# Performance work log

Measured on AMD Instinct MI355X. Metric: run time of the kernel, lower is better.

Reference implementation:

```python
import jax, jax.numpy as jnp
import numpy as np

EMB = 192
HEADS = 6
WIN = (8, 8)
N = WIN[0] * WIN[1]  # 64
B_ = 2048
NW = 1024  # mask windows per image; B_ % NW == 0


def _relative_position_index():
    coords_h = np.arange(WIN[0])
    coords_w = np.arange(WIN[1])
    coords = np.stack(np.meshgrid(coords_h, coords_w, indexing='ij'))  # (2,Wh,Ww)
    cf = coords.reshape(2, -1)
    rel = cf[:, :, None] - cf[:, None, :]  # (2,N,N)
    rel = rel.transpose(1, 2, 0)
    rel[:, :, 0] += WIN[0] - 1
    rel[:, :, 1] += WIN[1] - 1
    rel[:, :, 0] *= 2 * WIN[1] - 1
    return rel.sum(-1).astype(np.int32)  # (N,N)


def setup_inputs() -> dict:
    key = jax.random.key(0)
    ks = jax.random.split(key, 12)
    num_bias = (2 * WIN[0] - 1) * (2 * WIN[1] - 1)  # 225
    s = 0.02
    return {
        'q': jax.random.normal(ks[0], (B_, N, EMB), jnp.float32),
        'k': jax.random.normal(ks[1], (B_, N, EMB), jnp.float32),
        'v': jax.random.normal(ks[2], (B_, N, EMB), jnp.float32),
        'mask': jax.random.normal(ks[3], (NW, N, N), jnp.float32),
        'Wq': jax.random.normal(ks[4], (EMB, EMB), jnp.float32) * s,
        'bq': jnp.zeros((EMB,), jnp.float32),
        'Wk': jax.random.normal(ks[5], (EMB, EMB), jnp.float32) * s,
        'bk': jnp.zeros((EMB,), jnp.float32),
        'Wv': jax.random.normal(ks[6], (EMB, EMB), jnp.float32) * s,
        'bv': jnp.zeros((EMB,), jnp.float32),
        'Wp': jax.random.normal(ks[7], (EMB, EMB), jnp.float32) * s,
        'bp': jnp.zeros((EMB,), jnp.float32),
        'bias_table': jax.random.normal(ks[8], (num_bias, HEADS), jnp.float32) * s,
        'rel_index': jnp.asarray(_relative_position_index()),
    }


def reference(q, k, v, mask, Wq, bq, Wk, bk, Wv, bv, Wp, bp, bias_table, rel_index):
    head_dim = EMB // HEADS
    scale = head_dim ** -0.5

    def split_heads(x):
        # (B_,N,C) -> (B_,H,N,D)
        return x.reshape(B_, N, HEADS, head_dim).transpose(0, 2, 1, 3)

    qh = split_heads(q @ Wq + bq) * scale
    kh = split_heads(k @ Wk + bk)
    vh = split_heads(v @ Wv + bv)

    attn = jnp.einsum('bhnd,bhmd->bhnm', qh, kh)  # (B_,H,N,N)

    # gathered relative position bias: (N,N,H) -> (H,N,N)
    rel_bias = bias_table[rel_index.reshape(-1)].reshape(N, N, HEADS).transpose(2, 0, 1)
    attn = attn + rel_bias[None]

    # mask add: reshape to (B, nW, H, N, N) and broadcast mask over batch/heads
    nW = mask.shape[0]
    attn = attn.reshape(-1, nW, HEADS, N, N) + mask[None, :, None]
    attn = attn.reshape(-1, HEADS, N, N)
    attn = jax.nn.softmax(attn, axis=-1)

    x = jnp.einsum('bhnm,bhmd->bhnd', attn, vh)  # (B_,H,N,D)
    x = x.transpose(0, 2, 1, 3).reshape(B_, N, EMB)
    x = x @ Wp + bp
    return (x, attn)
```

## Files before the change

kernel.cpp:

```cpp
#include <hip/hip_runtime.h>
#include <hip/hip_bf16.h>

typedef __attribute__((ext_vector_type(8))) short   bf16x8;
typedef __attribute__((ext_vector_type(4))) float   f32x4;
typedef unsigned short u16;

#define NTOK 64
#define CEMB 192
#define NH   6
#define ROWB 384
#define VROWB 128

__device__ __forceinline__ u16 f2b(float f) {
  unsigned u = __float_as_uint(f);
  unsigned r = (u + 0x7fffu + ((u >> 16) & 1u)) >> 16;
  return (u16)r;
}

__device__ __forceinline__ unsigned cvtpk(float lo, float hi) {
  unsigned r;
  asm("v_cvt_pk_bf16_f32 %0, %1, %2" : "=v"(r) : "v"(lo), "v"(hi));
  return r;
}

__device__ __forceinline__ int swz(int row, int colbyte) {
  return colbyte ^ ((((row >> 3) ^ row) & 7) << 4);
}

__global__ void prep_kernel(const float* __restrict__ Wq, const float* __restrict__ Wk,
                            const float* __restrict__ Wv, const float* __restrict__ Wp,
                            const float* __restrict__ btab, const int* __restrict__ ridx,
                            u16* __restrict__ WT, float* __restrict__ rb) {
  int idx = blockIdx.x * 256 + threadIdx.x;
  if (idx < 4 * 36864) {
    int m = idx / 36864;
    int e = idx - m * 36864;
    int n = e / CEMB;
    int k = e - n * CEMB;
    const float* W = (m == 0) ? Wq : (m == 1) ? Wk : (m == 2) ? Wv : Wp;
    WT[idx] = f2b(W[k * CEMB + n]);
  } else {
    int i2 = idx - 4 * 36864;
    if (i2 < NH * 4096) {
      int h = i2 >> 12;
      int ij = i2 & 4095;
      rb[i2] = btab[ridx[ij] * NH + h];
    }
  }
}

__global__ __launch_bounds__(512, 4)
void wattn_kernel(const float* __restrict__ qg, const float* __restrict__ kg,
                  const float* __restrict__ vg, const float* __restrict__ maskg,
                  const float* __restrict__ bq, const float* __restrict__ bk,
                  const float* __restrict__ bv, const float* __restrict__ bp,
                  const u16* __restrict__ WT, const float* __restrict__ rb,
                  float* __restrict__ xout, float* __restrict__ attn_out) {
  __shared__ __align__(16) char smem[81920];
  char* sQ = smem;
  char* sK = smem + 24576;
  char* sV = smem + 49152;
  const int tid  = threadIdx.x;
  const int wave = tid >> 6;
  const int lane = tid & 63;
  const int l15  = lane & 15;
  const int lhi  = lane >> 4;
  char* sP = smem + 73728 + wave * 1024;
  const int b = blockIdx.x;
  const float scale = 0.17677669529663687f;

  {
    const size_t base = (size_t)b * NTOK * CEMB;
    #pragma unroll
    for (int m = 0; m < 3; ++m) {
      const float* src = (m == 0 ? qg : m == 1 ? kg : vg) + base;
      char* dst = (m == 0 ? sQ : m == 1 ? sK : sV);
      #pragma unroll
      for (int it = 0; it < 6; ++it) {
        int fi  = it * 512 + tid;
        int row = fi / 48;
        int ce  = (fi - row * 48) * 4;
        const float4 v4 = reinterpret_cast<const float4*>(src)[fi];
        uint2 w;
        w.x = cvtpk(v4.x, v4.y);
        w.y = cvtpk(v4.z, v4.w);
        *reinterpret_cast<uint2*>(dst + row * ROWB + swz(row, ce * 2)) = w;
      }
    }
  }
  __syncthreads();

  #pragma unroll
  for (int m = 0; m < 3; ++m) {
    const char* Xs = (m == 0) ? sQ : (m == 1) ? sK : sV;
    const float* bias = (m == 0) ? bq : (m == 1) ? bk : bv;
    f32x4 acc[2][4];
    #pragma unroll
    for (int si = 0; si < 2; ++si) {
      int strip = wave + si * 8;
      if (strip < 12) {
        const u16* Wt = WT + m * 36864 + (strip * 16 + l15) * CEMB + lhi * 8;
        #pragma unroll
        for (int rt = 0; rt < 4; ++rt) { f32x4 z = {0.f,0.f,0.f,0.f}; acc[si][rt] = z; }
        #pragma unroll
        for (int ks = 0; ks < 6; ++ks) {
          bf16x8 bw = *reinterpret_cast<const bf16x8*>(Wt + ks * 32);
          #pragma unroll
          for (int rt = 0; rt < 4; ++rt) {
            int row = rt * 16 + l15;
            bf16x8 ax = *reinterpret_cast<const bf16x8*>(Xs + row * ROWB + swz(row, ks * 64 + lhi * 16));
            acc[si][rt] = __builtin_amdgcn_mfma_f32_16x16x32_bf16(ax, bw, acc[si][rt], 0, 0, 0);
          }
        }
      }
    }
    __syncthreads();
    #pragma unroll
    for (int si = 0; si < 2; ++si) {
      int strip = wave + si * 8;
      if (strip < 12) {
        int c = strip * 16 + l15;
        float bval = bias[c];
        if (m == 0) {
          #pragma unroll
          for (int rt = 0; rt < 4; ++rt)
            #pragma unroll
            for (int r = 0; r < 4; ++r) {
              int row = rt * 16 + lhi * 4 + r;
              *reinterpret_cast<u16*>(sQ + row * ROWB + swz(row, c * 2)) = f2b((acc[si][rt][r] + bval) * scale);
            }
        } else if (m == 1) {
          #pragma unroll
          for (int rt = 0; rt < 4; ++rt)
            #pragma unroll
            for (int r = 0; r < 4; ++r) {
              int row = rt * 16 + lhi * 4 + r;
              *reinterpret_cast<u16*>(sK + row * ROWB + swz(row, c * 2)) = f2b(acc[si][rt][r] + bval);
            }
        } else {
          #pragma unroll
          for (int rt = 0; rt < 4; ++rt) {
            int t0 = rt * 16 + lhi * 4;
            uint2 w;
            w.x = cvtpk(acc[si][rt][0] + bval, acc[si][rt][1] + bval);
            w.y = cvtpk(acc[si][rt][2] + bval, acc[si][rt][3] + bval);
            *reinterpret_cast<uint2*>(sV + c * VROWB + swz(c, t0 * 2)) = w;
          }
        }
      }
    }
  }
  __syncthreads();

  const float* maskw = maskg + (size_t)(b & 1023) * 4096;
  const int rt   = wave & 3;
  const int qrow = rt * 16 + l15;
  const int irow = rt * 16 + lhi * 4;

  f32x4 mk4[4];
  #pragma unroll
  for (int ct = 0; ct < 4; ++ct)
    mk4[ct] = *reinterpret_cast<const f32x4*>(maskw + qrow * 64 + ct * 16 + lhi * 4);

  #pragma unroll
  for (int ui = 0; ui < 3; ++ui) {
    int u = wave + ui * 8;
    int h = u >> 2;

    f32x4 rb4[4];
    #pragma unroll
    for (int ct = 0; ct < 4; ++ct)
      rb4[ct] = *reinterpret_cast<const f32x4*>(rb + h * 4096 + qrow * 64 + ct * 16 + lhi * 4);

    bf16x8 aq = *reinterpret_cast<const bf16x8*>(sQ + qrow * ROWB + swz(qrow, h * 64 + lhi * 16));
    f32x4 sv[4];
    #pragma unroll
    for (int ct = 0; ct < 4; ++ct) {
      int krow = ct * 16 + l15;
      bf16x8 bkf = *reinterpret_cast<const bf16x8*>(sK + krow * ROWB + swz(krow, h * 64 + lhi * 16));
      f32x4 z = {0.f, 0.f, 0.f, 0.f};
      sv[ct] = __builtin_amdgcn_mfma_f32_16x16x32_bf16(bkf, aq, z, 0, 0, 0);
    }

    float lg[4][4];
    #pragma unroll
    for (int ct = 0; ct < 4; ++ct)
      #pragma unroll
      for (int r = 0; r < 4; ++r)
        lg[ct][r] = sv[ct][r] + rb4[ct][r] + mk4[ct][r];

    float mx = fmaxf(fmaxf(fmaxf(lg[0][0], lg[0][1]), fmaxf(lg[0][2], lg[0][3])),
                     fmaxf(fmaxf(lg[1][0], lg[1][1]), fmaxf(lg[1][2], lg[1][3])));
    mx = fmaxf(mx, fmaxf(fmaxf(fmaxf(lg[2][0], lg[2][1]), fmaxf(lg[2][2], lg[2][3])),
                         fmaxf(fmaxf(lg[3][0], lg[3][1]), fmaxf(lg[3][2], lg[3][3]))));
    mx = fmaxf(mx, __shfl_xor(mx, 16));
    mx = fmaxf(mx, __shfl_xor(mx, 32));

    float e[4][4];
    float sum = 0.f;
    #pragma unroll
    for (int ct = 0; ct < 4; ++ct)
      #pragma unroll
      for (int r = 0; r < 4; ++r) {
        e[ct][r] = __expf(lg[ct][r] - mx);
        sum += e[ct][r];
      }
    sum += __shfl_xor(sum, 16);
    sum += __shfl_xor(sum, 32);
    float inv = 1.0f / sum;

    float pr[4][4];
    #pragma unroll
    for (int ct = 0; ct < 4; ++ct)
      #pragma unroll
      for (int r = 0; r < 4; ++r)
        pr[ct][r] = e[ct][r] * inv;

    float* ap = attn_out + ((size_t)b * NH + h) * 4096 + qrow * 64;
    #pragma unroll
    for (int ct = 0; ct < 4; ++ct) {
      f32x4 p4;
      p4[0] = pr[ct][0]; p4[1] = pr[ct][1]; p4[2] = pr[ct][2]; p4[3] = pr[ct][3];
      *reinterpret_cast<f32x4*>(ap + ct * 16 + lhi * 4) = p4;
    }

    f32x4 xa[2];
    { f32x4 z = {0.f, 0.f, 0.f, 0.f}; xa[0] = z; xa[1] = z; }
    #pragma unroll
    for (int ks = 0; ks < 2; ++ks) {
      #pragma unroll
      for (int c = 0; c < 2; ++c) {
        int ct = ks * 2 + c;
        int kg = c * 2 + (lhi >> 1);
        uint2 w;
        w.x = cvtpk(pr[ct][0], pr[ct][1]);
        w.y = cvtpk(pr[ct][2], pr[ct][3]);
        *reinterpret_cast<uint2*>(sP + (kg * 16 + l15) * 16 + (lhi & 1) * 8) = w;
      }
      bf16x8 apf = *reinterpret_cast<const bf16x8*>(sP + lane * 16);
      #pragma unroll
      for (int ctv = 0; ctv < 2; ++ctv) {
        int vrow = h * 32 + ctv * 16 + l15;
        bf16x8 bvf = *reinterpret_cast<const bf16x8*>(sV + vrow * VROWB + swz(vrow, ks * 64 + lhi * 16));
        xa[ctv] = __builtin_amdgcn_mfma_f32_16x16x32_bf16(apf, bvf, xa[ctv], 0, 0, 0);
      }
    }

    #pragma unroll
    for (int ctv = 0; ctv < 2; ++ctv)
      #pragma unroll
      for (int r = 0; r < 4; ++r) {
        int xrow = irow + r;
        int xcol = h * 32 + ctv * 16 + l15;
        *reinterpret_cast<u16*>(sQ + xrow * ROWB + swz(xrow, xcol * 2)) = f2b(xa[ctv][r]);
      }
  }
  __syncthreads();

  #pragma unroll
  for (int ui = 0; ui < 3; ++ui) {
    int u2 = wave + ui * 8;
    int ct = u2 % 12;
    int rh = u2 / 12;
    const u16* Wt = WT + 3 * 36864 + (ct * 16 + l15) * CEMB + lhi * 8;
    f32x4 oa[2];
    { f32x4 z = {0.f, 0.f, 0.f, 0.f}; oa[0] = z; oa[1] = z; }
    #pragma unroll
    for (int ks = 0; ks < 6; ++ks) {
      bf16x8 bw = *reinterpret_cast<const bf16x8*>(Wt + ks * 32);
      #pragma unroll
      for (int rr = 0; rr < 2; ++rr) {
        int xrow = rh * 32 + rr * 16 + l15;
        bf16x8 ax = *reinterpret_cast<const bf16x8*>(sQ + xrow * ROWB + swz(xrow, ks * 64 + lhi * 16));
        oa[rr] = __builtin_amdgcn_mfma_f32_16x16x32_bf16(ax, bw, oa[rr], 0, 0, 0);
      }
    }
    float bias = bp[ct * 16 + l15];
    #pragma unroll
    for (int rr = 0; rr < 2; ++rr)
      #pragma unroll
      for (int r = 0; r < 4; ++r)
        xout[((size_t)b * NTOK + rh * 32 + rr * 16 + lhi * 4 + r) * CEMB + ct * 16 + l15] = oa[rr][r] + bias;
  }
}

extern "C" void kernel_launch(void* const* d_in, const int* in_sizes, int n_in,
                              void* d_out, int out_size, void* d_ws, size_t ws_size,
                              hipStream_t stream) {
  const float* q    = (const float*)d_in[0];
  const float* k    = (const float*)d_in[1];
  const float* v    = (const float*)d_in[2];
  const float* mask = (const float*)d_in[3];
  const float* Wq   = (const float*)d_in[4];
  const float* bq   = (const float*)d_in[5];
  const float* Wk   = (const float*)d_in[6];
  const float* bk   = (const float*)d_in[7];
  const float* Wv   = (const float*)d_in[8];
  const float* bv   = (const float*)d_in[9];
  const float* Wp   = (const float*)d_in[10];
  const float* bp   = (const float*)d_in[11];
  const float* btab = (const float*)d_in[12];
  const int*   ridx = (const int*)d_in[13];

  u16*   WT = (u16*)d_ws;
  float* rb = (float*)((char*)d_ws + 4 * 36864 * 2);

  float* xout = (float*)d_out;
  float* attn = xout + (size_t)2048 * NTOK * CEMB;

  prep_kernel<<<672, 256, 0, stream>>>(Wq, Wk, Wv, Wp, btab, ridx, WT, rb);
  wattn_kernel<<<2048, 512, 0, stream>>>(q, k, v, mask, bq, bk, bv, bp, WT, rb, xout, attn);
}
```

Baseline: 214.0 us.

## Shrink LDS to two buffers, keep Q in registers, drop P scratch

Reorganizes the fused window-attention kernel so that LDS drops from three Q/K/V buffers plus per-wave P scratch to two 24KB buffers. Q is projected transposed straight into registers as bf16 fragments, and K is prefetched into registers and staged after Q. Scores and P·V now use 16x16x16 MFMAs, so the P fragments come straight from the accumulator layout without an LDS round trip. The aim is higher occupancy (launch bounds raised to 6) and fewer LDS writes, at the cost of extra barriers, including one inside the head loop, and more register pressure.

```diff
diff --git a/kernel.cpp b/kernel.cpp
--- a/kernel.cpp
+++ b/kernel.cpp
@@ -2,6 +2,7 @@
 #include <hip/hip_bf16.h>
 
 typedef __attribute__((ext_vector_type(8))) short   bf16x8;
+typedef __attribute__((ext_vector_type(4))) short   bf16x4;
 typedef __attribute__((ext_vector_type(4))) float   f32x4;
 typedef unsigned short u16;
 
@@ -26,6 +27,12 @@
 __device__ __forceinline__ int swz(int row, int colbyte) {
   return colbyte ^ ((((row >> 3) ^ row) & 7) << 4);
 }
+
+__device__ __forceinline__ f32x4 mfma16(bf16x4 a, bf16x4 b, f32x4 c) {
+  return __builtin_amdgcn_mfma_f32_16x16x16bf16_1k(a, b, c, 0, 0, 0);
+}
+
+union PK2 { unsigned u[2]; bf16x4 v; };
 
 __global__ void prep_kernel(const float* __restrict__ Wq, const float* __restrict__ Wk,
                             const float* __restrict__ Wv, const float* __restrict__ Wp,
@@ -49,67 +56,105 @@
   }
 }
 
-__global__ __launch_bounds__(512, 4)
+__global__ __launch_bounds__(512, 6)
 void wattn_kernel(const float* __restrict__ qg, const float* __restrict__ kg,
                   const float* __restrict__ vg, const float* __restrict__ maskg,
                   const float* __restrict__ bq, const float* __restrict__ bk,
                   const float* __restrict__ bv, const float* __restrict__ bp,
                   const u16* __restrict__ WT, const float* __restrict__ rb,
                   float* __restrict__ xout, float* __restrict__ attn_out) {
-  __shared__ __align__(16) char smem[81920];
-  char* sQ = smem;
-  char* sK = smem + 24576;
-  char* sV = smem + 49152;
+  __shared__ __align__(16) char smem[49152];
+  char* bA = smem;
+  char* bB = smem + 24576;
   const int tid  = threadIdx.x;
   const int wave = tid >> 6;
   const int lane = tid & 63;
   const int l15  = lane & 15;
   const int lhi  = lane >> 4;
-  char* sP = smem + 73728 + wave * 1024;
-  const int b = blockIdx.x;
+  const int b    = blockIdx.x;
+  const int rt   = wave & 3;
+  const int p    = wave >> 2;
   const float scale = 0.17677669529663687f;
 
+  const size_t base = (size_t)b * NTOK * CEMB;
+
+  #pragma unroll
+  for (int it = 0; it < 6; ++it) {
+    int fi  = it * 512 + tid;
+    int row = fi / 48;
+    int ce  = (fi - row * 48) * 4;
+    float4 v4 = reinterpret_cast<const float4*>(qg + base)[fi];
+    uint2 w;
+    w.x = cvtpk(v4.x, v4.y); w.y = cvtpk(v4.z, v4.w);
+    *reinterpret_cast<uint2*>(bA + row * ROWB + swz(row, ce * 2)) = w;
+    float4 v5 = reinterpret_cast<const float4*>(vg + base)[fi];
+    uint2 w2;
+    w2.x = cvtpk(v5.x, v5.y); w2.y = cvtpk(v5.z, v5.w);
+    *reinterpret_cast<uint2*>(bB + row * ROWB + swz(row, ce * 2)) = w2;
+  }
+  __syncthreads();
+
+  float4 kreg[6];
+  #pragma unroll
+  for (int it = 0; it < 6; ++it)
+    kreg[it] = reinterpret_cast<const float4*>(kg + base)[it * 512 + tid];
+
+  bf16x4 qb[6];
   {
-    const size_t base = (size_t)b * NTOK * CEMB;
-    #pragma unroll
-    for (int m = 0; m < 3; ++m) {
-      const float* src = (m == 0 ? qg : m == 1 ? kg : vg) + base;
-      char* dst = (m == 0 ? sQ : m == 1 ? sK : sV);
-      #pragma unroll
-      for (int it = 0; it < 6; ++it) {
-        int fi  = it * 512 + tid;
-        int row = fi / 48;
-        int ce  = (fi - row * 48) * 4;
-        const float4 v4 = reinterpret_cast<const float4*>(src)[fi];
-        uint2 w;
-        w.x = cvtpk(v4.x, v4.y);
-        w.y = cvtpk(v4.z, v4.w);
-        *reinterpret_cast<uint2*>(dst + row * ROWB + swz(row, ce * 2)) = w;
-      }
-    }
-  }
-  __syncthreads();
-
-  #pragma unroll
-  for (int m = 0; m < 3; ++m) {
-    const char* Xs = (m == 0) ? sQ : (m == 1) ? sK : sV;
-    const float* bias = (m == 0) ? bq : (m == 1) ? bk : bv;
+    f32x4 qa[6];
+    #pragma unroll
+    for (int s6 = 0; s6 < 6; ++s6) { f32x4 z = {0.f,0.f,0.f,0.f}; qa[s6] = z; }
+    int row = rt * 16 + l15;
+    #pragma unroll
+    for (int ks = 0; ks < 6; ++ks) {
+      bf16x8 ax = *reinterpret_cast<const bf16x8*>(bA + row * ROWB + swz(row, ks * 64 + lhi * 16));
+      #pragma unroll
+      for (int s6 = 0; s6 < 6; ++s6) {
+        int strip = (p + (s6 >> 1) * 2) * 2 + (s6 & 1);
+        bf16x8 bw = *reinterpret_cast<const bf16x8*>(WT + (strip * 16 + l15) * CEMB + ks * 32 + lhi * 8);
+        qa[s6] = __builtin_amdgcn_mfma_f32_16x16x32_bf16(bw, ax, qa[s6], 0, 0, 0);
+      }
+    }
+    #pragma unroll
+    for (int s6 = 0; s6 < 6; ++s6) {
+      int strip = (p + (s6 >> 1) * 2) * 2 + (s6 & 1);
+      f32x4 b4 = *reinterpret_cast<const f32x4*>(bq + strip * 16 + lhi * 4);
+      PK2 pk;
+      pk.u[0] = cvtpk((qa[s6][0] + b4[0]) * scale, (qa[s6][1] + b4[1]) * scale);
+      pk.u[1] = cvtpk((qa[s6][2] + b4[2]) * scale, (qa[s6][3] + b4[3]) * scale);
+      qb[s6] = pk.v;
+    }
+  }
+  __syncthreads();
+
+  #pragma unroll
+  for (int it = 0; it < 6; ++it) {
+    int fi  = it * 512 + tid;
+    int row = fi / 48;
+    int ce  = (fi - row * 48) * 4;
+    uint2 w;
+    w.x = cvtpk(kreg[it].x, kreg[it].y); w.y = cvtpk(kreg[it].z, kreg[it].w);
+    *reinterpret_cast<uint2*>(bA + row * ROWB + swz(row, ce * 2)) = w;
+  }
+  __syncthreads();
+
+  {
     f32x4 acc[2][4];
     #pragma unroll
     for (int si = 0; si < 2; ++si) {
       int strip = wave + si * 8;
       if (strip < 12) {
-        const u16* Wt = WT + m * 36864 + (strip * 16 + l15) * CEMB + lhi * 8;
-        #pragma unroll
-        for (int rt = 0; rt < 4; ++rt) { f32x4 z = {0.f,0.f,0.f,0.f}; acc[si][rt] = z; }
+        const u16* Wt = WT + 36864 + (strip * 16 + l15) * CEMB + lhi * 8;
+        #pragma unroll
+        for (int r2 = 0; r2 < 4; ++r2) { f32x4 z = {0.f,0.f,0.f,0.f}; acc[si][r2] = z; }
         #pragma unroll
         for (int ks = 0; ks < 6; ++ks) {
           bf16x8 bw = *reinterpret_cast<const bf16x8*>(Wt + ks * 32);
           #pragma unroll
-          for (int rt = 0; rt < 4; ++rt) {
-            int row = rt * 16 + l15;
-            bf16x8 ax = *reinterpret_cast<const bf16x8*>(Xs + row * ROWB + swz(row, ks * 64 + lhi * 16));
-            acc[si][rt] = __builtin_amdgcn_mfma_f32_16x16x32_bf16(ax, bw, acc[si][rt], 0, 0, 0);
+          for (int r2 = 0; r2 < 4; ++r2) {
+            int row = r2 * 16 + l15;
+            bf16x8 ax = *reinterpret_cast<const bf16x8*>(bA + row * ROWB + swz(row, ks * 64 + lhi * 16));
+            acc[si][r2] = __builtin_amdgcn_mfma_f32_16x16x32_bf16(ax, bw, acc[si][r2], 0, 0, 0);
           }
         }
       }
@@ -120,139 +165,132 @@
       int strip = wave + si * 8;
       if (strip < 12) {
         int c = strip * 16 + l15;
-        float bval = bias[c];
-        if (m == 0) {
+        float bval = bk[c];
+        #pragma unroll
+        for (int r2 = 0; r2 < 4; ++r2)
           #pragma unroll
-          for (int rt = 0; rt < 4; ++rt)
-            #pragma unroll
-            for (int r = 0; r < 4; ++r) {
-              int row = rt * 16 + lhi * 4 + r;
-              *reinterpret_cast<u16*>(sQ + row * ROWB + swz(row, c * 2)) = f2b((acc[si][rt][r] + bval) * scale);
-            }
-        } else if (m == 1) {
+          for (int r = 0; r < 4; ++r) {
+            int row = r2 * 16 + lhi * 4 + r;
+            *reinterpret_cast<u16*>(bA + row * ROWB + swz(row, c * 2)) = f2b(acc[si][r2][r] + bval);
+          }
+      }
+    }
+  }
+
+  {
+    f32x4 acc[2][4];
+    #pragma unroll
+    for (int si = 0; si < 2; ++si) {
+      int strip = wave + si * 8;
+      if (strip < 12) {
+        const u16* Wt = WT + 2 * 36864 + (strip * 16 + l15) * CEMB + lhi * 8;
+        #pragma unroll
+        for (int r2 = 0; r2 < 4; ++r2) { f32x4 z = {0.f,0.f,0.f,0.f}; acc[si][r2] = z; }
+        #pragma unroll
+        for (int ks = 0; ks < 6; ++ks) {
+          bf16x8 bw = *reinterpret_cast<const bf16x8*>(Wt + ks * 32);
           #pragma unroll
-          for (int rt = 0; rt < 4; ++rt)
-            #pragma unroll
-            for (int r = 0; r < 4; ++r) {
-              int row = rt * 16 + lhi * 4 + r;
-              *reinterpret_cast<u16*>(sK + row * ROWB + swz(row, c * 2)) = f2b(acc[si][rt][r] + bval);
-            }
-        } else {
-          #pragma unroll
-          for (int rt = 0; rt < 4; ++rt) {
-            int t0 = rt * 16 + lhi * 4;
-            uint2 w;
-            w.x = cvtpk(acc[si][rt][0] + bval, acc[si][rt][1] + bval);
-            w.y = cvtpk(acc[si][rt][2] + bval, acc[si][rt][3] + bval);
-            *reinterpret_cast<uint2*>(sV + c * VROWB + swz(c, t0 * 2)) = w;
+          for (int r2 = 0; r2 < 4; ++r2) {
+            int row = r2 * 16 + l15;
+            bf16x8 ax = *reinterpret_cast<const bf16x8*>(bB + row * ROWB + swz(row, ks * 64 + lhi * 16));
+            acc[si][r2] = __builtin_amdgcn_mfma_f32_16x16x32_bf16(ax, bw, acc[si][r2], 0, 0, 0);
           }
         }
       }
     }
+    __syncthreads();
+    #pragma unroll
+    for (int si = 0; si < 2; ++si) {
+      int strip = wave + si * 8;
+      if (strip < 12) {
+        int c = strip * 16 + l15;
+        float bval = bv[c];
+        #pragma unroll
+        for (int r2 = 0; r2 < 4; ++r2) {
+          int t0 = r2 * 16 + lhi * 4;
+          uint2 w;
+          w.x = cvtpk(acc[si][r2][0] + bval, acc[si][r2][1] + bval);
+          w.y = cvtpk(acc[si][r2][2] + bval, acc[si][r2][3] + bval);
+          *reinterpret_cast<uint2*>(bB + c * VROWB + swz(c, t0 * 2)) = w;
+        }
+      }
+    }
   }
   __syncthreads();
 
   const float* maskw = maskg + (size_t)(b & 1023) * 4096;
-  const int rt   = wave & 3;
   const int qrow = rt * 16 + l15;
-  const int irow = rt * 16 + lhi * 4;
-
-  f32x4 mk4[4];
-  #pragma unroll
-  for (int ct = 0; ct < 4; ++ct)
-    mk4[ct] = *reinterpret_cast<const f32x4*>(maskw + qrow * 64 + ct * 16 + lhi * 4);
 
   #pragma unroll
   for (int ui = 0; ui < 3; ++ui) {
-    int u = wave + ui * 8;
-    int h = u >> 2;
-
-    f32x4 rb4[4];
-    #pragma unroll
-    for (int ct = 0; ct < 4; ++ct)
-      rb4[ct] = *reinterpret_cast<const f32x4*>(rb + h * 4096 + qrow * 64 + ct * 16 + lhi * 4);
-
-    bf16x8 aq = *reinterpret_cast<const bf16x8*>(sQ + qrow * ROWB + swz(qrow, h * 64 + lhi * 16));
-    f32x4 sv[4];
+    int h = 2 * ui + p;
+
+    f32x4 lg4[4];
     #pragma unroll
     for (int ct = 0; ct < 4; ++ct) {
       int krow = ct * 16 + l15;
-      bf16x8 bkf = *reinterpret_cast<const bf16x8*>(sK + krow * ROWB + swz(krow, h * 64 + lhi * 16));
+      bf16x4 a0 = *reinterpret_cast<const bf16x4*>(bA + krow * ROWB + swz(krow, h * 64 + lhi * 8));
+      bf16x4 a1 = *reinterpret_cast<const bf16x4*>(bA + krow * ROWB + swz(krow, h * 64 + 32 + lhi * 8));
       f32x4 z = {0.f, 0.f, 0.f, 0.f};
-      sv[ct] = __builtin_amdgcn_mfma_f32_16x16x32_bf16(bkf, aq, z, 0, 0, 0);
-    }
-
-    float lg[4][4];
-    #pragma unroll
-    for (int ct = 0; ct < 4; ++ct)
-      #pragma unroll
-      for (int r = 0; r < 4; ++r)
-        lg[ct][r] = sv[ct][r] + rb4[ct][r] + mk4[ct][r];
-
-    float mx = fmaxf(fmaxf(fmaxf(lg[0][0], lg[0][1]), fmaxf(lg[0][2], lg[0][3])),
-                     fmaxf(fmaxf(lg[1][0], lg[1][1]), fmaxf(lg[1][2], lg[1][3])));
-    mx = fmaxf(mx, fmaxf(fmaxf(fmaxf(lg[2][0], lg[2][1]), fmaxf(lg[2][2], lg[2][3])),
-                         fmaxf(fmaxf(lg[3][0], lg[3][1]), fmaxf(lg[3][2], lg[3][3]))));
+      f32x4 s = mfma16(a0, qb[2 * ui], z);
+      s = mfma16(a1, qb[2 * ui + 1], s);
+      f32x4 r4 = *reinterpret_cast<const f32x4*>(rb + h * 4096 + qrow * 64 + ct * 16 + lhi * 4);
+      f32x4 m4 = *reinterpret_cast<const f32x4*>(maskw + qrow * 64 + ct * 16 + lhi * 4);
+      #pragma unroll
+      for (int r = 0; r < 4; ++r) lg4[ct][r] = s[r] + r4[r] + m4[r];
+    }
+
+    float mx = fmaxf(fmaxf(fmaxf(lg4[0][0], lg4[0][1]), fmaxf(lg4[0][2], lg4[0][3])),
+                     fmaxf(fmaxf(lg4[1][0], lg4[1][1]), fmaxf(lg4[1][2], lg4[1][3])));
+    mx = fmaxf(mx, fmaxf(fmaxf(fmaxf(lg4[2][0], lg4[2][1]), fmaxf(lg4[2][2], lg4[2][3])),
+                         fmaxf(fmaxf(lg4[3][0], lg4[3][1]), fmaxf(lg4[3][2], lg4[3][3]))));
     mx = fmaxf(mx, __shfl_xor(mx, 16));
     mx = fmaxf(mx, __shfl_xor(mx, 32));
 
-    float e[4][4];
     float sum = 0.f;
     #pragma unroll
     for (int ct = 0; ct < 4; ++ct)
       #pragma unroll
       for (int r = 0; r < 4; ++r) {
-        e[ct][r] = __expf(lg[ct][r] - mx);
-        sum += e[ct][r];
+        lg4[ct][r] = __expf(lg4[ct][r] - mx);
+        sum += lg4[ct][r];
       }
     sum += __shfl_xor(sum, 16);
     sum += __shfl_xor(sum, 32);
     float inv = 1.0f / sum;
 
-    float pr[4][4];
-    #pragma unroll
-    for (int ct = 0; ct < 4; ++ct)
-      #pragma unroll
-      for (int r = 0; r < 4; ++r)
-        pr[ct][r] = e[ct][r] * inv;
-
     float* ap = attn_out + ((size_t)b * NH + h) * 4096 + qrow * 64;
+    PK2 pa[4];
     #pragma unroll
     for (int ct = 0; ct < 4; ++ct) {
       f32x4 p4;
-      p4[0] = pr[ct][0]; p4[1] = pr[ct][1]; p4[2] = pr[ct][2]; p4[3] = pr[ct][3];
+      #pragma unroll
+      for (int r = 0; r < 4; ++r) p4[r] = lg4[ct][r] * inv;
       *reinterpret_cast<f32x4*>(ap + ct * 16 + lhi * 4) = p4;
+      pa[ct].u[0] = cvtpk(p4[0], p4[1]);
+      pa[ct].u[1] = cvtpk(p4[2], p4[3]);
     }
 
     f32x4 xa[2];
     { f32x4 z = {0.f, 0.f, 0.f, 0.f}; xa[0] = z; xa[1] = z; }
     #pragma unroll
-    for (int ks = 0; ks < 2; ++ks) {
-      #pragma unroll
-      for (int c = 0; c < 2; ++c) {
-        int ct = ks * 2 + c;
-        int kg = c * 2 + (lhi >> 1);
-        uint2 w;
-        w.x = cvtpk(pr[ct][0], pr[ct][1]);
-        w.y = cvtpk(pr[ct][2], pr[ct][3]);
-        *reinterpret_cast<uint2*>(sP + (kg * 16 + l15) * 16 + (lhi & 1) * 8) = w;
-      }
-      bf16x8 apf = *reinterpret_cast<const bf16x8*>(sP + lane * 16);
-      #pragma unroll
-      for (int ctv = 0; ctv < 2; ++ctv) {
-        int vrow = h * 32 + ctv * 16 + l15;
-        bf16x8 bvf = *reinterpret_cast<const bf16x8*>(sV + vrow * VROWB + swz(vrow, ks * 64 + lhi * 16));
-        xa[ctv] = __builtin_amdgcn_mfma_f32_16x16x32_bf16(apf, bvf, xa[ctv], 0, 0, 0);
-      }
-    }
+    for (int ctv = 0; ctv < 2; ++ctv) {
+      int vrow = h * 32 + ctv * 16 + l15;
+      #pragma unroll
+      for (int ct = 0; ct < 4; ++ct) {
+        bf16x4 bvf = *reinterpret_cast<const bf16x4*>(bB + vrow * VROWB + swz(vrow, ct * 32 + lhi * 8));
+        xa[ctv] = mfma16(pa[ct].v, bvf, xa[ctv]);
+      }
+    }
+    __syncthreads();
 
     #pragma unroll
     for (int ctv = 0; ctv < 2; ++ctv)
       #pragma unroll
       for (int r = 0; r < 4; ++r) {
-        int xrow = irow + r;
+        int xrow = rt * 16 + lhi * 4 + r;
         int xcol = h * 32 + ctv * 16 + l15;
-        *reinterpret_cast<u16*>(sQ + xrow * ROWB + swz(xrow, xcol * 2)) = f2b(xa[ctv][r]);
+        *reinterpret_cast<u16*>(bA + xrow * ROWB + swz(xrow, xcol * 2)) = f2b(xa[ctv][r]);
       }
   }
   __syncthreads();
@@ -271,7 +309,7 @@
       #pragma unroll
       for (int rr = 0; rr < 2; ++rr) {
         int xrow = rh * 32 + rr * 16 + l15;
-        bf16x8 ax = *reinterpret_cast<const bf16x8*>(sQ + xrow * ROWB + swz(xrow, ks * 64 + lhi * 16));
+        bf16x8 ax = *reinterpret_cast<const bf16x8*>(bA + xrow * ROWB + swz(xrow, ks * 64 + lhi * 16));
         oa[rr] = __builtin_amdgcn_mfma_f32_16x16x32_bf16(ax, bw, oa[rr], 0, 0, 0);
       }
     }
```

Measured after the change: 276.5 us. 1.29x slower.
